# Performance work log

Measured on AMD Instinct MI355X. Metric: run time of the kernel, lower is better.

## Reference

```python
import jax, jax.numpy as jnp
import numpy as np

N_NODES = 100000
N_EDGES = 1600000
K_HOPS = 10


def setup_inputs() -> dict:
    key = jax.random.key(0)
    ks = jax.random.split(key, 8)
    x = jax.random.normal(ks[0], (N_NODES, 512), dtype=jnp.float32)
    edge_src = jax.random.randint(ks[1], (N_EDGES,), 0, N_NODES, dtype=jnp.int32)
    edge_dst = jax.random.randint(ks[2], (N_EDGES,), 0, N_NODES, dtype=jnp.int32)
    # positive, roughly degree-normalized edge weights (stand-in for sym-normalized adj)
    edge_weight = jax.random.uniform(ks[3], (N_EDGES,), dtype=jnp.float32) / 16.0
    node_index = jax.random.randint(ks[4], (10000,), 0, N_NODES, dtype=jnp.int32)
    W1 = jax.random.normal(ks[5], (512, 64), dtype=jnp.float32) * 0.05
    W2 = jax.random.normal(ks[6], (64, 64), dtype=jnp.float32) * 0.05
    w_prop = jax.random.normal(ks[7], (64, 1), dtype=jnp.float32) * 0.05
    return {"x": x, "edge_src": edge_src, "edge_dst": edge_dst,
            "edge_weight": edge_weight, "node_index": node_index,
            "W1": W1, "W2": W2, "w_prop": w_prop}


def reference(x, edge_src, edge_dst, edge_weight, node_index, W1, W2, w_prop):
    # MLP (dropout is identity at inference, use_bias=False)
    h = jax.nn.relu(x @ W1)          # [N, 64]
    h = jax.nn.relu(h @ W2)          # [N, C]

    # K-hop sparse propagation: h_{k+1} = A @ h_k via edge-list SpMM
    def spmm(v):
        return jax.ops.segment_sum(edge_weight[:, None] * v[edge_src],
                                   edge_dst, num_segments=N_NODES)

    props = [h]
    cur = h
    for _ in range(K_HOPS):
        cur = spmm(cur)
        props.append(cur)
    H = jnp.stack(props, axis=1)     # [N, K+1, C]

    # sigmoid-gated combination across hops (DAGNN)
    score = jax.nn.sigmoid(H @ w_prop)        # [N, K+1, 1]
    out = jnp.sum(score * H, axis=1)          # [N, C]

    # gather requested nodes
    return out[node_index]                    # [n_idx, C]
```

## Files before the change

### kernel.cpp

```cpp
#include <hip/hip_runtime.h>
#include <hip/hip_bf16.h>

#define C 64

__device__ __forceinline__ float b2f(unsigned short s) {
    return __uint_as_float(((unsigned int)s) << 16);
}
__device__ __forceinline__ unsigned short f2b(float f) {
    unsigned int u = __float_as_uint(f);
    u = (u + 0x7FFF + ((u >> 16) & 1)) >> 16;
    return (unsigned short)u;
}
__device__ __forceinline__ float4 bf4(ushort4 u) {
    return make_float4(b2f(u.x), b2f(u.y), b2f(u.z), b2f(u.w));
}

__launch_bounds__(256)
__global__ void mlp_kernel(const float* __restrict__ x,
                           const float* __restrict__ W1,
                           const float* __restrict__ W2,
                           float* __restrict__ h0,
                           unsigned short* __restrict__ hb, int nN)
{
    __shared__ float smem[8704];
    float (*As)[68] = (float(*)[68])smem;
    float (*Bs)[68] = (float(*)[68])(smem + 4352);
    float (*Hs)[68] = (float(*)[68])smem;
    float (*Ws)[68] = (float(*)[68])(smem + 4352);

    const int t  = threadIdx.x;
    const int ty = t >> 4;
    const int tx = t & 15;
    const int row0 = blockIdx.x * 64;

    const int srow = t >> 4;
    const int slk  = (t & 15) * 4;

    float acc[4][4] = {};

    for (int k0 = 0; k0 < 512; k0 += 64) {
        #pragma unroll
        for (int h = 0; h < 4; ++h) {
            int r = srow + 16 * h;
            int grow = row0 + r;
            float4 v = make_float4(0.f, 0.f, 0.f, 0.f);
            if (grow < nN) v = *(const float4*)&x[(size_t)grow * 512 + k0 + slk];
            *(float4*)&As[r][slk] = v;
        }
        #pragma unroll
        for (int h = 0; h < 4; ++h) {
            int r = srow + 16 * h;
            *(float4*)&Bs[r][slk] = *(const float4*)&W1[(size_t)(k0 + r) * 64 + slk];
        }
        __syncthreads();

        for (int kk = 0; kk < 64; kk += 4) {
            float4 b0 = *(float4*)&Bs[kk + 0][tx * 4];
            float4 b1 = *(float4*)&Bs[kk + 1][tx * 4];
            float4 b2 = *(float4*)&Bs[kk + 2][tx * 4];
            float4 b3 = *(float4*)&Bs[kk + 3][tx * 4];
            #pragma unroll
            for (int i = 0; i < 4; ++i) {
                float4 a = *(float4*)&As[ty * 4 + i][kk];
                acc[i][0] += a.x * b0.x + a.y * b1.x + a.z * b2.x + a.w * b3.x;
                acc[i][1] += a.x * b0.y + a.y * b1.y + a.z * b2.y + a.w * b3.y;
                acc[i][2] += a.x * b0.z + a.y * b1.z + a.z * b2.z + a.w * b3.z;
                acc[i][3] += a.x * b0.w + a.y * b1.w + a.z * b2.w + a.w * b3.w;
            }
        }
        __syncthreads();
    }

    #pragma unroll
    for (int i = 0; i < 4; ++i) {
        float4 o;
        o.x = acc[i][0] > 0.f ? acc[i][0] : 0.f;
        o.y = acc[i][1] > 0.f ? acc[i][1] : 0.f;
        o.z = acc[i][2] > 0.f ? acc[i][2] : 0.f;
        o.w = acc[i][3] > 0.f ? acc[i][3] : 0.f;
        *(float4*)&Hs[ty * 4 + i][tx * 4] = o;
    }
    #pragma unroll
    for (int q = 0; q < 4; ++q) {
        int r = srow + 16 * q;
        *(float4*)&Ws[r][slk] = *(const float4*)&W2[(size_t)r * 64 + slk];
    }
    __syncthreads();

    float acc2[4][4] = {};
    for (int kk = 0; kk < 64; kk += 4) {
        float4 b0 = *(float4*)&Ws[kk + 0][tx * 4];
        float4 b1 = *(float4*)&Ws[kk + 1][tx * 4];
        float4 b2 = *(float4*)&Ws[kk + 2][tx * 4];
        float4 b3 = *(float4*)&Ws[kk + 3][tx * 4];
        #pragma unroll
        for (int i = 0; i < 4; ++i) {
            float4 a = *(float4*)&Hs[ty * 4 + i][kk];
            acc2[i][0] += a.x * b0.x + a.y * b1.x + a.z * b2.x + a.w * b3.x;
            acc2[i][1] += a.x * b0.y + a.y * b1.y + a.z * b2.y + a.w * b3.y;
            acc2[i][2] += a.x * b0.z + a.y * b1.z + a.z * b2.z + a.w * b3.z;
            acc2[i][3] += a.x * b0.w + a.y * b1.w + a.z * b2.w + a.w * b3.w;
        }
    }

    #pragma unroll
    for (int i = 0; i < 4; ++i) {
        int grow = row0 + ty * 4 + i;
        if (grow < nN) {
            float4 o;
            o.x = acc2[i][0] > 0.f ? acc2[i][0] : 0.f;
            o.y = acc2[i][1] > 0.f ? acc2[i][1] : 0.f;
            o.z = acc2[i][2] > 0.f ? acc2[i][2] : 0.f;
            o.w = acc2[i][3] > 0.f ? acc2[i][3] : 0.f;
            *(float4*)&h0[(size_t)grow * 64 + tx * 4] = o;
            ushort4 ob = make_ushort4(f2b(o.x), f2b(o.y), f2b(o.z), f2b(o.w));
            *(ushort4*)&hb[(size_t)grow * 64 + tx * 4] = ob;
        }
    }
}

__launch_bounds__(256)
__global__ void count_kernel(const int* __restrict__ dst, int* __restrict__ rowptr, int nE)
{
    int e = blockIdx.x * 256 + threadIdx.x;
    if (e < nE) atomicAdd(&rowptr[dst[e]], 1);
}

__launch_bounds__(1024)
__global__ void scan_kernel(int* __restrict__ deg, int nN)
{
    __shared__ int sums[1024];
    const int t = threadIdx.x;
    const int len = (nN + 1023) / 1024;
    const int lo = t * len;
    const int hi = min(nN, lo + len);
    int s = 0;
    for (int i = lo; i < hi; ++i) s += deg[i];
    sums[t] = s;
    __syncthreads();
    for (int d = 1; d < 1024; d <<= 1) {
        int v = (t >= d) ? sums[t - d] : 0;
        __syncthreads();
        sums[t] += v;
        __syncthreads();
    }
    int off = sums[t] - s;
    for (int i = lo; i < hi; ++i) {
        int d = deg[i];
        deg[i] = off;
        off += d;
    }
}

__launch_bounds__(256)
__global__ void fill_kernel(const int* __restrict__ src, const int* __restrict__ dst,
                            const float* __restrict__ w,
                            int* __restrict__ rowptr,
                            int2* __restrict__ cwp, int nE)
{
    int e = blockIdx.x * 256 + threadIdx.x;
    if (e >= nE) return;
    int d = dst[e];
    int pos = atomicAdd(&rowptr[d], 1);
    cwp[pos] = make_int2(src[e], __float_as_int(w[e]));
}

__launch_bounds__(256)
__global__ void spmm_fused(const int* __restrict__ rowptr,
                           const int2* __restrict__ cwp,
                           const unsigned short* __restrict__ cur,
                           unsigned short* __restrict__ nxt,
                           const int* __restrict__ idx,
                           const float* __restrict__ wp,
                           float* __restrict__ out,
                           int nN, int nI, int nodeBlocks)
{
    const int bid  = blockIdx.x;
    const int wid  = threadIdx.x >> 6;
    const int lane = threadIdx.x & 63;
    const int g = lane >> 4;
    const int q = lane & 15;

    int node, oi = -1;
    if (bid < nodeBlocks) {
        node = bid * 4 + wid;
        if (node >= nN) return;
    } else {
        oi = (bid - nodeBlocks) * 4 + wid;
        if (oi >= nI) return;
        node = idx[oi];
    }

    const int beg = (node == 0) ? 0 : rowptr[node - 1];
    const int end = rowptr[node];

    float4 A0 = make_float4(0.f,0.f,0.f,0.f);
    float4 A1 = make_float4(0.f,0.f,0.f,0.f);
    float4 A2 = make_float4(0.f,0.f,0.f,0.f);
    float4 A3 = make_float4(0.f,0.f,0.f,0.f);

    for (int e0 = beg; e0 < end; e0 += 64) {
        int el = e0 + lane;
        int2 ce = make_int2(0, 0);
        if (el < end) ce = cwp[el];
        int rem = end - e0; if (rem > 64) rem = 64;

        for (int s0 = 0; s0 < rem; s0 += 16) {
            int s = s0 + g;
            int   c0 = __shfl(ce.x, s);
            float w0 = __int_as_float(__shfl(ce.y, s));
            int   c1 = __shfl(ce.x, s + 4);
            float w1 = __int_as_float(__shfl(ce.y, s + 4));
            int   c2 = __shfl(ce.x, s + 8);
            float w2 = __int_as_float(__shfl(ce.y, s + 8));
            int   c3 = __shfl(ce.x, s + 12);
            float w3 = __int_as_float(__shfl(ce.y, s + 12));
            float4 v0 = bf4(*(const ushort4*)&cur[(size_t)c0 * 64 + q * 4]);
            float4 v1 = bf4(*(const ushort4*)&cur[(size_t)c1 * 64 + q * 4]);
            float4 v2 = bf4(*(const ushort4*)&cur[(size_t)c2 * 64 + q * 4]);
            float4 v3 = bf4(*(const ushort4*)&cur[(size_t)c3 * 64 + q * 4]);
            A0.x += w0*v0.x; A0.y += w0*v0.y; A0.z += w0*v0.z; A0.w += w0*v0.w;
            A1.x += w1*v1.x; A1.y += w1*v1.y; A1.z += w1*v1.z; A1.w += w1*v1.w;
            A2.x += w2*v2.x; A2.y += w2*v2.y; A2.z += w2*v2.z; A2.w += w2*v2.w;
            A3.x += w3*v3.x; A3.y += w3*v3.y; A3.z += w3*v3.z; A3.w += w3*v3.w;
        }
    }
    A0.x += A1.x + A2.x + A3.x;
    A0.y += A1.y + A2.y + A3.y;
    A0.z += A1.z + A2.z + A3.z;
    A0.w += A1.w + A2.w + A3.w;

    A0.x += __shfl_xor(A0.x, 16); A0.y += __shfl_xor(A0.y, 16);
    A0.z += __shfl_xor(A0.z, 16); A0.w += __shfl_xor(A0.w, 16);
    A0.x += __shfl_xor(A0.x, 32); A0.y += __shfl_xor(A0.y, 32);
    A0.z += __shfl_xor(A0.z, 32); A0.w += __shfl_xor(A0.w, 32);

    if (oi < 0) {
        if (g == 0) {
            ushort4 ob = make_ushort4(f2b(A0.x), f2b(A0.y), f2b(A0.z), f2b(A0.w));
            *(ushort4*)&nxt[(size_t)node * 64 + q * 4] = ob;
        }
    } else {
        float s = A0.x * wp[q * 4] + A0.y * wp[q * 4 + 1]
                + A0.z * wp[q * 4 + 2] + A0.w * wp[q * 4 + 3];
        s += __shfl_xor(s, 1); s += __shfl_xor(s, 2);
        s += __shfl_xor(s, 4); s += __shfl_xor(s, 8);
        float gate = 1.f / (1.f + __expf(-s));
        if (g == 0) {
            float* op = &out[(size_t)oi * 64 + q * 4];
            float4 prev = *(float4*)op;
            prev.x += gate * A0.x; prev.y += gate * A0.y;
            prev.z += gate * A0.z; prev.w += gate * A0.w;
            *(float4*)op = prev;
        }
    }
}

__launch_bounds__(256)
__global__ void gate_gather(const float* __restrict__ h,
                            const int* __restrict__ idx,
                            const float* __restrict__ wp,
                            float* __restrict__ out, int nI)
{
    int gid = blockIdx.x * 256 + threadIdx.x;
    int i = gid >> 6;
    if (i >= nI) return;
    int c = gid & 63;
    int n = idx[i];
    float v = h[(size_t)n * 64 + c];
    float s = v * wp[c];
    #pragma unroll
    for (int off = 32; off > 0; off >>= 1)
        s += __shfl_xor(s, off);
    float gate = 1.f / (1.f + __expf(-s));
    out[gid] = gate * v;
}

extern "C" void kernel_launch(void* const* d_in, const int* in_sizes, int n_in,
                              void* d_out, int out_size, void* d_ws, size_t ws_size,
                              hipStream_t stream) {
    const float* x    = (const float*)d_in[0];
    const int*   esrc = (const int*)d_in[1];
    const int*   edst = (const int*)d_in[2];
    const float* ew   = (const float*)d_in[3];
    const int*   nidx = (const int*)d_in[4];
    const float* W1   = (const float*)d_in[5];
    const float* W2   = (const float*)d_in[6];
    const float* wp   = (const float*)d_in[7];
    float* out = (float*)d_out;

    const int nN = in_sizes[0] / 512;
    const int nE = in_sizes[1];
    const int nI = in_sizes[4];

    float*          h0     = (float*)d_ws;
    unsigned short* bufA   = (unsigned short*)(h0 + (size_t)nN * C);
    unsigned short* bufB   = bufA + (size_t)nN * C;
    int*            rowptr = (int*)(bufB + (size_t)nN * C);
    int2*           cwp    = (int2*)(rowptr + nN);

    hipMemsetAsync(rowptr, 0, (size_t)nN * sizeof(int), stream);
    count_kernel<<<(nE + 255) / 256, 256, 0, stream>>>(edst, rowptr, nE);
    scan_kernel<<<1, 1024, 0, stream>>>(rowptr, nN);
    fill_kernel<<<(nE + 255) / 256, 256, 0, stream>>>(esrc, edst, ew, rowptr, cwp, nE);

    mlp_kernel<<<(nN + 63) / 64, 256, 0, stream>>>(x, W1, W2, h0, bufA, nN);

    gate_gather<<<(nI * 64 + 255) / 256, 256, 0, stream>>>(h0, nidx, wp, out, nI);

    unsigned short* cur = bufA;
    unsigned short* nxt = bufB;
    const int nodeBlocks = (nN + 3) / 4;
    const int idxBlocks  = (nI + 3) / 4;
    for (int k = 0; k < 10; ++k) {
        const int nb = (k == 9) ? 0 : nodeBlocks;
        spmm_fused<<<nb + idxBlocks, 256, 0, stream>>>(
            rowptr, cwp, cur, nxt, nidx, wp, out, nN, nI, nb);
        unsigned short* tmp = cur; cur = nxt; nxt = tmp;
    }
}
```

Measured before the change: 1.086 ms.

## Parallelize CSR prefix scan and widen SpMM gathers to 16-byte bf16 loads

Replaces the single-block serial-chunk prefix scan over node degrees with a three-kernel block scan (per-block scan, scan of block sums, add offsets), using vectorized int4 accesses. The goal is to remove the long single-workgroup bottleneck in CSR construction. The SpMM kernel now has each lane load 8 bf16 values (16 bytes) per neighbor row instead of 4, so 8 neighbors are processed in parallel with 2 unrolled accumulators, and the bf16 unpacking is inlined. This trades fewer, wider memory transactions for more registers and one extra cross-lane reduction step. The block-sum buffer reuses bufB before that buffer is written.

```diff
diff --git a/kernel.cpp b/kernel.cpp
--- a/kernel.cpp
+++ b/kernel.cpp
@@ -10,9 +10,6 @@
     unsigned int u = __float_as_uint(f);
     u = (u + 0x7FFF + ((u >> 16) & 1)) >> 16;
     return (unsigned short)u;
-}
-__device__ __forceinline__ float4 bf4(ushort4 u) {
-    return make_float4(b2f(u.x), b2f(u.y), b2f(u.z), b2f(u.w));
 }
 
 __launch_bounds__(256)
@@ -81,8 +78,8 @@
         *(float4*)&Hs[ty * 4 + i][tx * 4] = o;
     }
     #pragma unroll
-    for (int q = 0; q < 4; ++q) {
-        int r = srow + 16 * q;
+    for (int qq = 0; qq < 4; ++qq) {
+        int r = srow + 16 * qq;
         *(float4*)&Ws[r][slk] = *(const float4*)&W2[(size_t)r * 64 + slk];
     }
     __syncthreads();
@@ -126,29 +123,75 @@
     if (e < nE) atomicAdd(&rowptr[dst[e]], 1);
 }
 
-__launch_bounds__(1024)
-__global__ void scan_kernel(int* __restrict__ deg, int nN)
-{
-    __shared__ int sums[1024];
+__launch_bounds__(256)
+__global__ void scanA(int* __restrict__ deg, int* __restrict__ bsum, int nN)
+{
+    __shared__ int ts[256];
     const int t = threadIdx.x;
-    const int len = (nN + 1023) / 1024;
-    const int lo = t * len;
-    const int hi = min(nN, lo + len);
-    int s = 0;
-    for (int i = lo; i < hi; ++i) s += deg[i];
-    sums[t] = s;
+    const int base = blockIdx.x * 1024 + t * 4;
+    int v0 = 0, v1 = 0, v2 = 0, v3 = 0;
+    if (base + 3 < nN) {
+        int4 v = *(const int4*)&deg[base];
+        v0 = v.x; v1 = v.y; v2 = v.z; v3 = v.w;
+    } else {
+        if (base + 0 < nN) v0 = deg[base + 0];
+        if (base + 1 < nN) v1 = deg[base + 1];
+        if (base + 2 < nN) v2 = deg[base + 2];
+        if (base + 3 < nN) v3 = deg[base + 3];
+    }
+    int s = v0 + v1 + v2 + v3;
+    ts[t] = s;
     __syncthreads();
-    for (int d = 1; d < 1024; d <<= 1) {
-        int v = (t >= d) ? sums[t - d] : 0;
-        __syncthreads();
-        sums[t] += v;
-        __syncthreads();
-    }
-    int off = sums[t] - s;
-    for (int i = lo; i < hi; ++i) {
-        int d = deg[i];
-        deg[i] = off;
-        off += d;
+    for (int d = 1; d < 256; d <<= 1) {
+        int xv = (t >= d) ? ts[t - d] : 0;
+        __syncthreads();
+        ts[t] += xv;
+        __syncthreads();
+    }
+    if (t == 255) bsum[blockIdx.x] = ts[255];
+    int e0 = ts[t] - s;
+    int e1 = e0 + v0;
+    int e2 = e1 + v1;
+    int e3 = e2 + v2;
+    if (base + 3 < nN) {
+        *(int4*)&deg[base] = make_int4(e0, e1, e2, e3);
+    } else {
+        if (base + 0 < nN) deg[base + 0] = e0;
+        if (base + 1 < nN) deg[base + 1] = e1;
+        if (base + 2 < nN) deg[base + 2] = e2;
+        if (base + 3 < nN) deg[base + 3] = e3;
+    }
+}
+
+__launch_bounds__(256)
+__global__ void scanB(int* __restrict__ bsum, int nB)
+{
+    __shared__ int ts[256];
+    const int t = threadIdx.x;
+    int v = (t < nB) ? bsum[t] : 0;
+    ts[t] = v;
+    __syncthreads();
+    for (int d = 1; d < 256; d <<= 1) {
+        int xv = (t >= d) ? ts[t - d] : 0;
+        __syncthreads();
+        ts[t] += xv;
+        __syncthreads();
+    }
+    if (t < nB) bsum[t] = ts[t] - v;
+}
+
+__launch_bounds__(256)
+__global__ void scanC(int* __restrict__ deg, const int* __restrict__ bsum, int nN)
+{
+    const int i4 = (blockIdx.x * 256 + threadIdx.x) * 4;
+    if (i4 >= nN) return;
+    const int b = bsum[i4 >> 10];
+    if (i4 + 3 < nN) {
+        int4 v = *(int4*)&deg[i4];
+        v.x += b; v.y += b; v.z += b; v.w += b;
+        *(int4*)&deg[i4] = v;
+    } else {
+        for (int j = 0; j < 4 && i4 + j < nN; ++j) deg[i4 + j] += b;
     }
 }
 
@@ -178,8 +221,8 @@
     const int bid  = blockIdx.x;
     const int wid  = threadIdx.x >> 6;
     const int lane = threadIdx.x & 63;
-    const int g = lane >> 4;
-    const int q = lane & 15;
+    const int g = lane >> 3;
+    const int q = lane & 7;
 
     int node, oi = -1;
     if (bid < nodeBlocks) {
@@ -194,10 +237,7 @@
     const int beg = (node == 0) ? 0 : rowptr[node - 1];
     const int end = rowptr[node];
 
-    float4 A0 = make_float4(0.f,0.f,0.f,0.f);
-    float4 A1 = make_float4(0.f,0.f,0.f,0.f);
-    float4 A2 = make_float4(0.f,0.f,0.f,0.f);
-    float4 A3 = make_float4(0.f,0.f,0.f,0.f);
+    float a0[8] = {}, a1[8] = {};
 
     for (int e0 = beg; e0 < end; e0 += 64) {
         int el = e0 + lane;
@@ -209,49 +249,63 @@
             int s = s0 + g;
             int   c0 = __shfl(ce.x, s);
             float w0 = __int_as_float(__shfl(ce.y, s));
-            int   c1 = __shfl(ce.x, s + 4);
-            float w1 = __int_as_float(__shfl(ce.y, s + 4));
-            int   c2 = __shfl(ce.x, s + 8);
-            float w2 = __int_as_float(__shfl(ce.y, s + 8));
-            int   c3 = __shfl(ce.x, s + 12);
-            float w3 = __int_as_float(__shfl(ce.y, s + 12));
-            float4 v0 = bf4(*(const ushort4*)&cur[(size_t)c0 * 64 + q * 4]);
-            float4 v1 = bf4(*(const ushort4*)&cur[(size_t)c1 * 64 + q * 4]);
-            float4 v2 = bf4(*(const ushort4*)&cur[(size_t)c2 * 64 + q * 4]);
-            float4 v3 = bf4(*(const ushort4*)&cur[(size_t)c3 * 64 + q * 4]);
-            A0.x += w0*v0.x; A0.y += w0*v0.y; A0.z += w0*v0.z; A0.w += w0*v0.w;
-            A1.x += w1*v1.x; A1.y += w1*v1.y; A1.z += w1*v1.z; A1.w += w1*v1.w;
-            A2.x += w2*v2.x; A2.y += w2*v2.y; A2.z += w2*v2.z; A2.w += w2*v2.w;
-            A3.x += w3*v3.x; A3.y += w3*v3.y; A3.z += w3*v3.z; A3.w += w3*v3.w;
-        }
-    }
-    A0.x += A1.x + A2.x + A3.x;
-    A0.y += A1.y + A2.y + A3.y;
-    A0.z += A1.z + A2.z + A3.z;
-    A0.w += A1.w + A2.w + A3.w;
-
-    A0.x += __shfl_xor(A0.x, 16); A0.y += __shfl_xor(A0.y, 16);
-    A0.z += __shfl_xor(A0.z, 16); A0.w += __shfl_xor(A0.w, 16);
-    A0.x += __shfl_xor(A0.x, 32); A0.y += __shfl_xor(A0.y, 32);
-    A0.z += __shfl_xor(A0.z, 32); A0.w += __shfl_xor(A0.w, 32);
+            int   c1 = __shfl(ce.x, s + 8);
+            float w1 = __int_as_float(__shfl(ce.y, s + 8));
+            int4 r0 = *(const int4*)&cur[(size_t)c0 * 64 + q * 8];
+            int4 r1 = *(const int4*)&cur[(size_t)c1 * 64 + q * 8];
+            a0[0] += w0 * __uint_as_float((unsigned)r0.x << 16);
+            a0[1] += w0 * __uint_as_float((unsigned)r0.x & 0xFFFF0000u);
+            a0[2] += w0 * __uint_as_float((unsigned)r0.y << 16);
+            a0[3] += w0 * __uint_as_float((unsigned)r0.y & 0xFFFF0000u);
+            a0[4] += w0 * __uint_as_float((unsigned)r0.z << 16);
+            a0[5] += w0 * __uint_as_float((unsigned)r0.z & 0xFFFF0000u);
+            a0[6] += w0 * __uint_as_float((unsigned)r0.w << 16);
+            a0[7] += w0 * __uint_as_float((unsigned)r0.w & 0xFFFF0000u);
+            a1[0] += w1 * __uint_as_float((unsigned)r1.x << 16);
+            a1[1] += w1 * __uint_as_float((unsigned)r1.x & 0xFFFF0000u);
+            a1[2] += w1 * __uint_as_float((unsigned)r1.y << 16);
+            a1[3] += w1 * __uint_as_float((unsigned)r1.y & 0xFFFF0000u);
+            a1[4] += w1 * __uint_as_float((unsigned)r1.z << 16);
+            a1[5] += w1 * __uint_as_float((unsigned)r1.z & 0xFFFF0000u);
+            a1[6] += w1 * __uint_as_float((unsigned)r1.w << 16);
+            a1[7] += w1 * __uint_as_float((unsigned)r1.w & 0xFFFF0000u);
+        }
+    }
+    #pragma unroll
+    for (int j = 0; j < 8; ++j) a0[j] += a1[j];
+
+    #pragma unroll
+    for (int j = 0; j < 8; ++j) {
+        a0[j] += __shfl_xor(a0[j], 8);
+        a0[j] += __shfl_xor(a0[j], 16);
+        a0[j] += __shfl_xor(a0[j], 32);
+    }
 
     if (oi < 0) {
         if (g == 0) {
-            ushort4 ob = make_ushort4(f2b(A0.x), f2b(A0.y), f2b(A0.z), f2b(A0.w));
-            *(ushort4*)&nxt[(size_t)node * 64 + q * 4] = ob;
-        }
-    } else {
-        float s = A0.x * wp[q * 4] + A0.y * wp[q * 4 + 1]
-                + A0.z * wp[q * 4 + 2] + A0.w * wp[q * 4 + 3];
-        s += __shfl_xor(s, 1); s += __shfl_xor(s, 2);
-        s += __shfl_xor(s, 4); s += __shfl_xor(s, 8);
+            int4 ob;
+            ob.x = (int)(((unsigned)f2b(a0[1]) << 16) | (unsigned)f2b(a0[0]));
+            ob.y = (int)(((unsigned)f2b(a0[3]) << 16) | (unsigned)f2b(a0[2]));
+            ob.z = (int)(((unsigned)f2b(a0[5]) << 16) | (unsigned)f2b(a0[4]));
+            ob.w = (int)(((unsigned)f2b(a0[7]) << 16) | (unsigned)f2b(a0[6]));
+            *(int4*)&nxt[(size_t)node * 64 + q * 8] = ob;
+        }
+    } else {
+        float s = 0.f;
+        #pragma unroll
+        for (int j = 0; j < 8; ++j) s += a0[j] * wp[q * 8 + j];
+        s += __shfl_xor(s, 1); s += __shfl_xor(s, 2); s += __shfl_xor(s, 4);
         float gate = 1.f / (1.f + __expf(-s));
         if (g == 0) {
-            float* op = &out[(size_t)oi * 64 + q * 4];
-            float4 prev = *(float4*)op;
-            prev.x += gate * A0.x; prev.y += gate * A0.y;
-            prev.z += gate * A0.z; prev.w += gate * A0.w;
-            *(float4*)op = prev;
+            float* op = &out[(size_t)oi * 64 + q * 8];
+            float4 p0 = *(float4*)op;
+            float4 p1 = *(float4*)(op + 4);
+            p0.x += gate * a0[0]; p0.y += gate * a0[1];
+            p0.z += gate * a0[2]; p0.w += gate * a0[3];
+            p1.x += gate * a0[4]; p1.y += gate * a0[5];
+            p1.z += gate * a0[6]; p1.w += gate * a0[7];
+            *(float4*)op = p0;
+            *(float4*)(op + 4) = p1;
         }
     }
 }
@@ -298,10 +352,15 @@
     unsigned short* bufB   = bufA + (size_t)nN * C;
     int*            rowptr = (int*)(bufB + (size_t)nN * C);
     int2*           cwp    = (int2*)(rowptr + nN);
+    int*            bsum   = (int*)bufB;
+
+    const int nB = (nN + 1023) / 1024;
 
     hipMemsetAsync(rowptr, 0, (size_t)nN * sizeof(int), stream);
     count_kernel<<<(nE + 255) / 256, 256, 0, stream>>>(edst, rowptr, nE);
-    scan_kernel<<<1, 1024, 0, stream>>>(rowptr, nN);
+    scanA<<<nB, 256, 0, stream>>>(rowptr, bsum, nN);
+    scanB<<<1, 256, 0, stream>>>(bsum, nB);
+    scanC<<<nB, 256, 0, stream>>>(rowptr, bsum, nN);
     fill_kernel<<<(nE + 255) / 256, 256, 0, stream>>>(esrc, edst, ew, rowptr, cwp, nE);
 
     mlp_kernel<<<(nN + 63) / 64, 256, 0, stream>>>(x, W1, W2, h0, bufA, nN);
```

Result: faster. 954.2 us (-12.1%).
